# Kernel optimization log

Measured on AMD Instinct MI355X. Metric: run time of the kernel, lower is better.

## Reference

```python
import jax, jax.numpy as jnp
import numpy as np

EMBED_DIM = 1024
NUM_HEADS = 16
HEAD_DIM = EMBED_DIM // NUM_HEADS
LN_EPS = 1e-5


def setup_inputs() -> dict:
    key = jax.random.key(0)
    ks = jax.random.split(key, 5)
    N, L, C = 32, 577, EMBED_DIM
    x = jax.random.normal(ks[0], (N, L, C), dtype=jnp.float32)
    ln1_g = jnp.ones((C,), dtype=jnp.float32)
    ln1_b = jnp.zeros((C,), dtype=jnp.float32)
    w_in = jax.random.normal(ks[1], (3 * C, C), dtype=jnp.float32) * (C ** -0.5)
    b_in = jax.random.normal(ks[2], (3 * C,), dtype=jnp.float32) * 0.02
    w_out = jax.random.normal(ks[3], (C, C), dtype=jnp.float32) * (C ** -0.5)
    b_out = jax.random.normal(ks[4], (C,), dtype=jnp.float32) * 0.02
    return {"x": x, "ln1_g": ln1_g, "ln1_b": ln1_b, "w_in": w_in,
            "b_in": b_in, "w_out": w_out, "b_out": b_out}


def _layernorm(x, g, b):
    mu = jnp.mean(x, axis=-1, keepdims=True)
    var = jnp.mean(jnp.square(x - mu), axis=-1, keepdims=True)
    return (x - mu) * jax.lax.rsqrt(var + LN_EPS) * g + b


def reference(x, ln1_g, ln1_b, w_in, b_in, w_out, b_out):
    # ClearCLIP last block, attn_variant='qq', keep_residual=False, keep_ffn=False.
    N, L, C = x.shape
    H, D = NUM_HEADS, HEAD_DIM
    z = _layernorm(x, ln1_g, ln1_b)
    qkv = z @ w_in.T + b_in                      # (N, L, 3C)
    q, k, v = jnp.split(qkv, 3, axis=-1)
    k = q                                        # 'qq' self-self variant
    def heads(t):
        return t.reshape(N, L, H, D).transpose(0, 2, 1, 3)  # (N, H, L, D)
    q, k, v = heads(q), heads(k), heads(v)
    scale = 1.0 / np.sqrt(D).astype(np.float32)
    scores = jnp.einsum('nhld,nhsd->nhls', q, k) * scale    # (N, H, L, L)
    attn = jax.nn.softmax(scores, axis=-1)
    out = jnp.einsum('nhls,nhsd->nhld', attn, v)            # (N, H, L, D)
    out = out.transpose(0, 2, 1, 3).reshape(N, L, C)
    return out @ w_out.T + b_out                 # ls_1 = Identity, no residual/FFN
```

## Files before the change

### kernel.cpp

```cpp
#include <hip/hip_runtime.h>
#include <stdint.h>

typedef short bf16x8 __attribute__((ext_vector_type(8)));
typedef float f32x4 __attribute__((ext_vector_type(4)));
typedef unsigned int uint4v __attribute__((ext_vector_type(4)));
typedef unsigned short ushort4v __attribute__((ext_vector_type(4)));
typedef float float4v __attribute__((ext_vector_type(4)));

#define MROWS 18464
#define SEQ   577
#define CDIM  1024
#define SPAD  640
#define W1ELEMS (2048*1024)
#define W2ELEMS (1024*1024)
#define SQC 0.42466089f

__device__ __forceinline__ unsigned short f2bf(float f) {
  unsigned int u = __float_as_uint(f);
  u += 0x7fffu + ((u >> 16) & 1u);
  return (unsigned short)(u >> 16);
}

__device__ __forceinline__ void load_lds16(const void* g, void* lds) {
  __builtin_amdgcn_global_load_lds(
      (const __attribute__((address_space(1))) unsigned int*)(uint64_t)(uintptr_t)g,
      (__attribute__((address_space(3))) unsigned int*)(unsigned int)(uintptr_t)lds,
      16, 0, 0);
}

__global__ __launch_bounds__(256) void ln_kernel(const float* __restrict__ x,
                                                 const float* __restrict__ g,
                                                 const float* __restrict__ b,
                                                 unsigned short* __restrict__ z) {
  const int row = blockIdx.x;
  const int t = threadIdx.x;
  const float4v v = *(const float4v*)(x + (size_t)row * CDIM + t * 4);
  float s  = v[0] + v[1] + v[2] + v[3];
  float ss = v[0]*v[0] + v[1]*v[1] + v[2]*v[2] + v[3]*v[3];
  #pragma unroll
  for (int off = 1; off < 64; off <<= 1) { s += __shfl_xor(s, off); ss += __shfl_xor(ss, off); }
  __shared__ float rs[4], rss[4];
  const int w = t >> 6, l = t & 63;
  if (l == 0) { rs[w] = s; rss[w] = ss; }
  __syncthreads();
  s = rs[0] + rs[1] + rs[2] + rs[3];
  ss = rss[0] + rss[1] + rss[2] + rss[3];
  const float mu = s * (1.0f / CDIM);
  const float var = ss * (1.0f / CDIM) - mu * mu;
  const float rstd = rsqrtf(var + 1e-5f);
  const float4v gv = *(const float4v*)(g + t * 4);
  const float4v bv = *(const float4v*)(b + t * 4);
  ushort4v o;
  #pragma unroll
  for (int j = 0; j < 4; ++j) o[j] = f2bf((v[j] - mu) * rstd * gv[j] + bv[j]);
  *(ushort4v*)(z + (size_t)row * CDIM + t * 4) = o;
}

__global__ __launch_bounds__(256) void conv_kernel(const float* __restrict__ w_in,
                                                   const float* __restrict__ w_out,
                                                   unsigned short* __restrict__ wqv,
                                                   unsigned short* __restrict__ wo,
                                                   unsigned short* __restrict__ vt) {
  const int idx = blockIdx.x * 256 + threadIdx.x;
  const int e = idx * 4;
  if (e < W1ELEMS) {
    const int row = e >> 10;
    const int srow = row < 1024 ? row : row + 1024;
    const float4v v = *(const float4v*)(w_in + (size_t)srow * 1024 + (e & 1023));
    ushort4v o;
    #pragma unroll
    for (int j = 0; j < 4; ++j) o[j] = f2bf(v[j]);
    *(ushort4v*)(wqv + e) = o;
  } else if (e < W1ELEMS + W2ELEMS) {
    const int e2 = e - W1ELEMS;
    const float4v v = *(const float4v*)(w_out + e2);
    ushort4v o;
    #pragma unroll
    for (int j = 0; j < 4; ++j) o[j] = f2bf(v[j]);
    *(ushort4v*)(wo + e2) = o;
  } else {
    const int pidx = idx - (W1ELEMS + W2ELEMS) / 4;
    const int ic = pidx >> 3, part = pidx & 7;
    *(uint4v*)(vt + (size_t)ic * SPAD + 576 + part * 8) = (uint4v)0u;
  }
}

__global__ __launch_bounds__(1024, 4) void gemm_qv(const unsigned short* __restrict__ A,
                                                   const unsigned short* __restrict__ B,
                                                   const float* __restrict__ bias,
                                                   unsigned short* __restrict__ qout,
                                                   unsigned short* __restrict__ vtout) {
  __shared__ char smem[131072];
  const int t = threadIdx.x;
  const int w = t >> 6, l = t & 63;
  const int L = (blockIdx.x & 7) * 73 + (blockIdx.x >> 3);
  const int p = L >> 3, c = L & 7;
  const int m0 = p * 256, n0 = c * 256;
  const int wm = w >> 2, wn = w & 3;
  const int g4 = (l >> 4) * 4;
  const int fr = l & 15;
  const int fb = (l >> 4) * 16;
  const int sw = (l & 7) << 4;

  f32x4 acc[4][4];
  #pragma unroll
  for (int i = 0; i < 4; ++i)
    #pragma unroll
    for (int j = 0; j < 4; ++j) acc[i][j] = (f32x4)0.0f;

  const int srow = l >> 3;
  const int scol = ((((l & 7) * 16) ^ ((srow & 7) << 4)) >> 1);
  int ra0 = m0 + w * 16 + srow;     if (ra0 > MROWS - 1) ra0 = MROWS - 1;
  int ra1 = m0 + w * 16 + 8 + srow; if (ra1 > MROWS - 1) ra1 = MROWS - 1;
  const unsigned short* pA0 = A + (size_t)ra0 * 1024 + scol;
  const unsigned short* pA1 = A + (size_t)ra1 * 1024 + scol;
  const unsigned short* pB0 = B + (size_t)(n0 + w * 16 + srow) * 1024 + scol;
  const unsigned short* pB1 = pB0 + (size_t)8 * 1024;

  #define STG(kt, buf)                                                     \
    {                                                                      \
      char* const dA_ = smem + (buf) * 65536 + w * 2048;                   \
      char* const dB_ = dA_ + 32768;                                       \
      const int k0_ = (kt) * 64;                                           \
      load_lds16(pA0 + k0_, dA_);                                          \
      load_lds16(pA1 + k0_, dA_ + 1024);                                   \
      load_lds16(pB0 + k0_, dB_);                                          \
      load_lds16(pB1 + k0_, dB_ + 1024);                                   \
    }

  STG(0, 0)
  __syncthreads();

  for (int kb = 0; kb < 16; ++kb) {
    const int b = kb & 1;
    if (kb < 15) STG(kb + 1, b ^ 1)
    const char* Ab = smem + b * 65536;
    const char* Bb = Ab + 32768;
    #pragma unroll
    for (int kk = 0; kk < 2; ++kk) {
      bf16x8 af[4], bfr[4];
      #pragma unroll
      for (int i = 0; i < 4; ++i)
        af[i] = *(const bf16x8*)(Ab + (wm * 64 + i * 16 + fr) * 128 + ((kk * 64 + fb) ^ sw));
      #pragma unroll
      for (int j = 0; j < 4; ++j)
        bfr[j] = *(const bf16x8*)(Bb + (wn * 64 + j * 16 + fr) * 128 + ((kk * 64 + fb) ^ sw));
      #pragma unroll
      for (int i = 0; i < 4; ++i)
        #pragma unroll
        for (int j = 0; j < 4; ++j)
          acc[i][j] = __builtin_amdgcn_mfma_f32_16x16x32_bf16(af[i], bfr[j], acc[i][j], 0, 0, 0);
    }
    __syncthreads();
  }
  #undef STG

  unsigned short* sm = (unsigned short*)smem;
  const bool isq = (n0 < 1024);
  const float* bb = isq ? (bias + n0) : (bias + 1024 + n0);
  const float scl = isq ? SQC : 1.0f;
  float bcol[4];
  #pragma unroll
  for (int j = 0; j < 4; ++j) bcol[j] = bb[wn * 64 + j * 16 + fr];
  for (int pass = 0; pass < 4; ++pass) {
    if (wm == pass) {
      #pragma unroll
      for (int i = 0; i < 4; ++i)
        #pragma unroll
        for (int j = 0; j < 4; ++j)
          #pragma unroll
          for (int r = 0; r < 4; ++r)
            sm[(i * 16 + g4 + r) * 264 + wn * 64 + j * 16 + fr] =
                f2bf((acc[i][j][r] + bcol[j]) * scl);
    }
    __syncthreads();
    if (isq) {
      #pragma unroll
      for (int it = 0; it < 2; ++it) {
        const int cid = it * 1024 + t;
        const int row = cid >> 5, ch = cid & 31;
        const int grow = m0 + pass * 64 + row;
        if (grow < MROWS)
          *(uint4v*)(qout + (size_t)grow * 1024 + n0 + ch * 8) =
              *(const uint4v*)(sm + row * 264 + ch * 8);
      }
    } else {
      const int tokloc = t & 63, chgrp = t >> 6;
      const int token = m0 + pass * 64 + tokloc;
      if (token < MROWS) {
        const unsigned int nimg = (unsigned int)token / 577u;
        const int s = token - (int)(nimg * 577u);
        unsigned short* op =
            vtout + ((size_t)nimg * 1024 + (n0 - 1024) + chgrp * 16) * SPAD + s;
        const unsigned short* sp = sm + tokloc * 264 + chgrp * 16;
        #pragma unroll 8
        for (int it = 0; it < 16; ++it)
          op[(size_t)it * SPAD] = sp[it];
      }
    }
    __syncthreads();
  }
}

__global__ __launch_bounds__(1024, 4) void gemm_proj(const unsigned short* __restrict__ A,
                                                     const unsigned short* __restrict__ B,
                                                     const float* __restrict__ bias,
                                                     float* __restrict__ outp) {
  __shared__ char smem[98304];
  const int t = threadIdx.x;
  const int w = t >> 6, l = t & 63;
  const int L = (blockIdx.x & 7) * 73 + (blockIdx.x >> 3);
  const int p = L >> 3, c = L & 7;
  const int m0 = p * 256, n0 = c * 128;
  const int wm = w >> 2, wn = w & 3;
  const int g4 = (l >> 4) * 4;
  const int fr = l & 15;
  const int fb = (l >> 4) * 16;
  const int sw = (l & 7) << 4;

  f32x4 acc[4][2];
  #pragma unroll
  for (int i = 0; i < 4; ++i)
    #pragma unroll
    for (int j = 0; j < 2; ++j) acc[i][j] = (f32x4)0.0f;

  const int srow = l >> 3;
  const int scol = ((((l & 7) * 16) ^ ((srow & 7) << 4)) >> 1);
  int ra0 = m0 + w * 16 + srow;     if (ra0 > MROWS - 1) ra0 = MROWS - 1;
  int ra1 = m0 + w * 16 + 8 + srow; if (ra1 > MROWS - 1) ra1 = MROWS - 1;
  const unsigned short* pA0 = A + (size_t)ra0 * 1024 + scol;
  const unsigned short* pA1 = A + (size_t)ra1 * 1024 + scol;
  const unsigned short* pB0 = B + (size_t)(n0 + w * 8 + srow) * 1024 + scol;

  #define STG(kt, buf)                                                     \
    {                                                                      \
      char* const dA_ = smem + (buf) * 49152 + w * 2048;                   \
      const int k0_ = (kt) * 64;                                           \
      load_lds16(pA0 + k0_, dA_);                                          \
      load_lds16(pA1 + k0_, dA_ + 1024);                                   \
      load_lds16(pB0 + k0_, smem + (buf) * 49152 + 32768 + w * 1024);      \
    }

  STG(0, 0)
  __syncthreads();

  for (int kb = 0; kb < 16; ++kb) {
    const int b = kb & 1;
    if (kb < 15) STG(kb + 1, b ^ 1)
    const char* Ab = smem + b * 49152;
    const char* Bb = Ab + 32768;
    #pragma unroll
    for (int kk = 0; kk < 2; ++kk) {
      bf16x8 af[4], bfr[2];
      #pragma unroll
      for (int i = 0; i < 4; ++i)
        af[i] = *(const bf16x8*)(Ab + (wm * 64 + i * 16 + fr) * 128 + ((kk * 64 + fb) ^ sw));
      #pragma unroll
      for (int j = 0; j < 2; ++j)
        bfr[j] = *(const bf16x8*)(Bb + (wn * 32 + j * 16 + fr) * 128 + ((kk * 64 + fb) ^ sw));
      #pragma unroll
      for (int i = 0; i < 4; ++i)
        #pragma unroll
        for (int j = 0; j < 2; ++j)
          acc[i][j] = __builtin_amdgcn_mfma_f32_16x16x32_bf16(af[i], bfr[j], acc[i][j], 0, 0, 0);
    }
    __syncthreads();
  }
  #undef STG

  float* smf = (float*)smem;
  float bcol[2];
  #pragma unroll
  for (int j = 0; j < 2; ++j) bcol[j] = bias[n0 + wn * 32 + j * 16 + fr];
  for (int q8 = 0; q8 < 8; ++q8) {
    if (wm == (q8 >> 1)) {
      const int i0 = (q8 & 1) * 2;
      #pragma unroll
      for (int i2 = 0; i2 < 2; ++i2)
        #pragma unroll
        for (int j = 0; j < 2; ++j)
          #pragma unroll
          for (int r = 0; r < 4; ++r)
            smf[(i2 * 16 + g4 + r) * 132 + wn * 32 + j * 16 + fr] =
                acc[i0 + i2][j][r] + bcol[j];
    }
    __syncthreads();
    {
      const int row = t >> 5, ch = t & 31;
      const int grow = m0 + q8 * 32 + row;
      if (grow < MROWS)
        *(float4v*)(outp + (size_t)grow * 1024 + n0 + ch * 4) =
            *(const float4v*)(smf + row * 132 + ch * 4);
    }
    __syncthreads();
  }
}

__global__ __launch_bounds__(256) void attn_kernel(const unsigned short* __restrict__ qbuf,
                                                   const unsigned short* __restrict__ vt,
                                                   unsigned short* __restrict__ out) {
  __shared__ char smem[32768];
  const int t = threadIdx.x, w = t >> 6, l = t & 63;
  const int g = l >> 4, fr = l & 15;
  const int bid = blockIdx.x;
  const int xcd = bid & 7, idx = bid >> 3;
  const int nhl = idx / 5;
  const int qb = idx - nhl * 5;
  const int nh = xcd * 64 + nhl;
  const int n = nh >> 4, h = nh & 15;
  const size_t rowbase = (size_t)n * SEQ;
  const int sw = (l & 7) << 4;

  bf16x8 bq[2][2];
  #pragma unroll
  for (int half = 0; half < 2; ++half) {
    const unsigned short* qp =
        qbuf + (rowbase + qb * 128 + half * 64 + w * 16 + fr) * 1024 + h * 64 + g * 8;
    bq[half][0] = *(const bf16x8*)qp;
    bq[half][1] = *(const bf16x8*)(qp + 32);
  }

  const int srow = l >> 3;
  const int scolE = ((((l & 7) * 16) ^ ((srow & 7) << 4)) >> 1);
  const unsigned short* ksrc = qbuf + (rowbase + w * 16 + srow) * 1024 + h * 64 + scolE;
  const unsigned short* vsrc = vt + ((size_t)nh * 64 + w * 16 + srow) * SPAD + scolE;

  f32x4 acc[2][4];
  #pragma unroll
  for (int half = 0; half < 2; ++half)
    #pragma unroll
    for (int cf = 0; cf < 4; ++cf) acc[half][cf] = (f32x4)0.0f;
  float l_run[2] = {0.0f, 0.0f};

  {
    char* kdst = smem + (w * 16) * 128;
    char* vdst = smem + 8192 + (w * 16) * 128;
    load_lds16(ksrc, kdst);
    load_lds16(ksrc + (size_t)8 * 1024, kdst + 1024);
    load_lds16(vsrc, vdst);
    load_lds16(vsrc + 8 * SPAD, vdst + 1024);
  }
  __syncthreads();

  for (int kb = 0; kb < 10; ++kb) {
    const int b = kb & 1;
    const char* kbuf = smem + b * 16384;
    const char* vbuf = kbuf + 8192;

    if (kb < 9) {
      char* kdst = smem + (b ^ 1) * 16384 + (w * 16) * 128;
      char* vdst = kdst + 8192;
      load_lds16(ksrc + (size_t)((kb + 1) * 64) * 1024, kdst);
      load_lds16(ksrc + (size_t)((kb + 1) * 64 + 8) * 1024, kdst + 1024);
      load_lds16(vsrc + (kb + 1) * 64, vdst);
      load_lds16(vsrc + 8 * SPAD + (kb + 1) * 64, vdst + 1024);
    }

    f32x4 s4[2][4];
    #pragma unroll
    for (int half = 0; half < 2; ++half)
      #pragma unroll
      for (int cf = 0; cf < 4; ++cf) s4[half][cf] = (f32x4)0.0f;
    #pragma unroll
    for (int kk = 0; kk < 2; ++kk)
      #pragma unroll
      for (int cf = 0; cf < 4; ++cf) {
        const bf16x8 af = *(const bf16x8*)(kbuf + (cf * 16 + fr) * 128 + ((kk * 64 + g * 16) ^ sw));
        s4[0][cf] = __builtin_amdgcn_mfma_f32_16x16x32_bf16(af, bq[0][kk], s4[0][cf], 0, 0, 0);
        s4[1][cf] = __builtin_amdgcn_mfma_f32_16x16x32_bf16(af, bq[1][kk], s4[1][cf], 0, 0, 0);
      }

    if (kb == 9) {
      #pragma unroll
      for (int half = 0; half < 2; ++half) {
        #pragma unroll
        for (int cf = 0; cf < 4; ++cf)
          #pragma unroll
          for (int r = 0; r < 4; ++r)
            if (cf != 0 || r != 0) s4[half][cf][r] = -__builtin_inff();
        s4[half][0][0] = (g == 0) ? s4[half][0][0] : -__builtin_inff();
      }
    }

    bf16x8 ap[2][2];
    #pragma unroll
    for (int half = 0; half < 2; ++half) {
      float sum = 0.0f;
      #pragma unroll
      for (int cf = 0; cf < 4; ++cf)
        #pragma unroll
        for (int r = 0; r < 4; ++r) {
          const float p2 = __builtin_amdgcn_exp2f(s4[half][cf][r]);
          s4[half][cf][r] = p2;
          sum += p2;
        }
      sum += __shfl_xor(sum, 16);
      sum += __shfl_xor(sum, 32);
      l_run[half] += sum;

      unsigned int pka[4], pkb[4];
      #pragma unroll
      for (int cf = 0; cf < 4; ++cf) {
        asm("v_cvt_pk_bf16_f32 %0, %1, %2" : "=v"(pka[cf]) : "v"(s4[half][cf][0]), "v"(s4[half][cf][1]));
        asm("v_cvt_pk_bf16_f32 %0, %1, %2" : "=v"(pkb[cf]) : "v"(s4[half][cf][2]), "v"(s4[half][cf][3]));
      }
      #pragma unroll
      for (int kk = 0; kk < 2; ++kk) {
        unsigned int a0 = pka[2 * kk], b0 = pka[2 * kk + 1];
        unsigned int a1 = pkb[2 * kk], b1 = pkb[2 * kk + 1];
        asm("v_permlane32_swap_b32 %0, %1" : "+v"(a0), "+v"(b0));
        asm("v_permlane16_swap_b32 %0, %1" : "+v"(a0), "+v"(b0));
        asm("v_permlane32_swap_b32 %0, %1" : "+v"(a1), "+v"(b1));
        asm("v_permlane16_swap_b32 %0, %1" : "+v"(a1), "+v"(b1));
        union { unsigned int i[4]; bf16x8 v; } u;
        u.i[0] = a0; u.i[1] = a1; u.i[2] = b0; u.i[3] = b1;
        ap[half][kk] = u.v;
      }
    }

    #pragma unroll
    for (int kk = 0; kk < 2; ++kk)
      #pragma unroll
      for (int cf = 0; cf < 4; ++cf) {
        const bf16x8 bv = *(const bf16x8*)(vbuf + (cf * 16 + fr) * 128 + ((kk * 64 + g * 16) ^ sw));
        acc[0][cf] = __builtin_amdgcn_mfma_f32_16x16x32_bf16(ap[0][kk], bv, acc[0][cf], 0, 0, 0);
        acc[1][cf] = __builtin_amdgcn_mfma_f32_16x16x32_bf16(ap[1][kk], bv, acc[1][cf], 0, 0, 0);
      }

    __syncthreads();
  }

  #pragma unroll
  for (int half = 0; half < 2; ++half) {
    const float rcp = 1.0f / l_run[half];
    #pragma unroll
    for (int r = 0; r < 4; ++r) {
      const float rr = __shfl(rcp, g * 4 + r);
      const int qg = qb * 128 + half * 64 + w * 16 + g * 4 + r;
      if (qg < SEQ) {
        #pragma unroll
        for (int cf = 0; cf < 4; ++cf)
          out[(rowbase + qg) * 1024 + h * 64 + cf * 16 + fr] = f2bf(acc[half][cf][r] * rr);
      }
    }
  }
}

extern "C" void kernel_launch(void* const* d_in, const int* in_sizes, int n_in,
                              void* d_out, int out_size, void* d_ws, size_t ws_size,
                              hipStream_t stream) {
  const float* x     = (const float*)d_in[0];
  const float* ln_g  = (const float*)d_in[1];
  const float* ln_b  = (const float*)d_in[2];
  const float* w_in  = (const float*)d_in[3];
  const float* b_in  = (const float*)d_in[4];
  const float* w_out = (const float*)d_in[5];
  const float* b_out = (const float*)d_in[6];

  unsigned short* z    = (unsigned short*)d_ws;
  unsigned short* qbuf = z + (size_t)MROWS * 1024;
  unsigned short* vt   = qbuf + (size_t)MROWS * 1024;
  unsigned short* wqv  = vt + (size_t)512 * 64 * SPAD;
  unsigned short* wo   = wqv + (size_t)2048 * 1024;

  ln_kernel<<<MROWS, 256, 0, stream>>>(x, ln_g, ln_b, z);
  conv_kernel<<<4096, 256, 0, stream>>>(w_in, w_out, wqv, wo, vt);
  gemm_qv<<<584, 1024, 0, stream>>>(z, wqv, b_in, qbuf, vt);
  attn_kernel<<<2560, 256, 0, stream>>>(qbuf, vt, z);
  gemm_proj<<<584, 1024, 0, stream>>>(z, wo, b_out, (float*)d_out);
}
```

Baseline: 243.4 us.

## Use 2-wave attention blocks with 64 query rows per wave and MFMA priority

The attention kernel drops from 4 to 2 waves per block. Each wave now handles 64 query rows (four 16-row groups) instead of 32, so every K/V fragment read from LDS feeds twice as many MFMAs, and each wave stages twice as many K/V rows per tile. The P·V step is interleaved per 16-row group, and the MFMA sections are wrapped in s_setprio raises. The cost is higher register pressure from 4x4 accumulators and score tiles, plus fewer waves per block to hide latency.

Measured after the change: 271.3 us. 11.5% more time.

```diff
diff --git a/kernel.cpp b/kernel.cpp
--- a/kernel.cpp
+++ b/kernel.cpp
@@ -296,7 +296,7 @@
   }
 }
 
-__global__ __launch_bounds__(256) void attn_kernel(const unsigned short* __restrict__ qbuf,
+__global__ __launch_bounds__(128) void attn_kernel(const unsigned short* __restrict__ qbuf,
                                                    const unsigned short* __restrict__ vt,
                                                    unsigned short* __restrict__ out) {
   __shared__ char smem[32768];
@@ -311,35 +311,39 @@
   const size_t rowbase = (size_t)n * SEQ;
   const int sw = (l & 7) << 4;
 
-  bf16x8 bq[2][2];
-  #pragma unroll
-  for (int half = 0; half < 2; ++half) {
+  bf16x8 bq[4][2];
+  #pragma unroll
+  for (int h2 = 0; h2 < 4; ++h2) {
     const unsigned short* qp =
-        qbuf + (rowbase + qb * 128 + half * 64 + w * 16 + fr) * 1024 + h * 64 + g * 8;
-    bq[half][0] = *(const bf16x8*)qp;
-    bq[half][1] = *(const bf16x8*)(qp + 32);
+        qbuf + (rowbase + qb * 128 + w * 64 + h2 * 16 + fr) * 1024 + h * 64 + g * 8;
+    bq[h2][0] = *(const bf16x8*)qp;
+    bq[h2][1] = *(const bf16x8*)(qp + 32);
   }
 
   const int srow = l >> 3;
   const int scolE = ((((l & 7) * 16) ^ ((srow & 7) << 4)) >> 1);
-  const unsigned short* ksrc = qbuf + (rowbase + w * 16 + srow) * 1024 + h * 64 + scolE;
-  const unsigned short* vsrc = vt + ((size_t)nh * 64 + w * 16 + srow) * SPAD + scolE;
-
-  f32x4 acc[2][4];
-  #pragma unroll
-  for (int half = 0; half < 2; ++half)
-    #pragma unroll
-    for (int cf = 0; cf < 4; ++cf) acc[half][cf] = (f32x4)0.0f;
-  float l_run[2] = {0.0f, 0.0f};
-
-  {
-    char* kdst = smem + (w * 16) * 128;
-    char* vdst = smem + 8192 + (w * 16) * 128;
-    load_lds16(ksrc, kdst);
-    load_lds16(ksrc + (size_t)8 * 1024, kdst + 1024);
-    load_lds16(vsrc, vdst);
-    load_lds16(vsrc + 8 * SPAD, vdst + 1024);
-  }
+  const unsigned short* ksrc = qbuf + (rowbase + w * 32 + srow) * 1024 + h * 64 + scolE;
+  const unsigned short* vsrc = vt + ((size_t)nh * 64 + w * 32 + srow) * SPAD + scolE;
+
+  f32x4 acc[4][4];
+  #pragma unroll
+  for (int h2 = 0; h2 < 4; ++h2)
+    #pragma unroll
+    for (int cf = 0; cf < 4; ++cf) acc[h2][cf] = (f32x4)0.0f;
+  float l_run[4] = {0.0f, 0.0f, 0.0f, 0.0f};
+
+  #define ASTG(kb_, buf_)                                                          \
+    {                                                                              \
+      char* kdst = smem + (buf_) * 16384 + (w * 32) * 128;                         \
+      char* vdst = kdst + 8192;                                                    \
+      _Pragma("unroll")                                                            \
+      for (int c2 = 0; c2 < 4; ++c2) {                                             \
+        load_lds16(ksrc + (size_t)((kb_) * 64 + c2 * 8) * 1024, kdst + c2 * 1024); \
+        load_lds16(vsrc + c2 * 8 * SPAD + (kb_) * 64, vdst + c2 * 1024);           \
+      }                                                                            \
+    }
+
+  ASTG(0, 0)
   __syncthreads();
 
   for (int kb = 0; kb < 10; ++kb) {
@@ -347,63 +351,59 @@
     const char* kbuf = smem + b * 16384;
     const char* vbuf = kbuf + 8192;
 
-    if (kb < 9) {
-      char* kdst = smem + (b ^ 1) * 16384 + (w * 16) * 128;
-      char* vdst = kdst + 8192;
-      load_lds16(ksrc + (size_t)((kb + 1) * 64) * 1024, kdst);
-      load_lds16(ksrc + (size_t)((kb + 1) * 64 + 8) * 1024, kdst + 1024);
-      load_lds16(vsrc + (kb + 1) * 64, vdst);
-      load_lds16(vsrc + 8 * SPAD + (kb + 1) * 64, vdst + 1024);
-    }
-
-    f32x4 s4[2][4];
-    #pragma unroll
-    for (int half = 0; half < 2; ++half)
-      #pragma unroll
-      for (int cf = 0; cf < 4; ++cf) s4[half][cf] = (f32x4)0.0f;
+    if (kb < 9) ASTG(kb + 1, b ^ 1)
+
+    f32x4 s4[4][4];
+    #pragma unroll
+    for (int h2 = 0; h2 < 4; ++h2)
+      #pragma unroll
+      for (int cf = 0; cf < 4; ++cf) s4[h2][cf] = (f32x4)0.0f;
+    __builtin_amdgcn_s_setprio(1);
     #pragma unroll
     for (int kk = 0; kk < 2; ++kk)
       #pragma unroll
       for (int cf = 0; cf < 4; ++cf) {
         const bf16x8 af = *(const bf16x8*)(kbuf + (cf * 16 + fr) * 128 + ((kk * 64 + g * 16) ^ sw));
-        s4[0][cf] = __builtin_amdgcn_mfma_f32_16x16x32_bf16(af, bq[0][kk], s4[0][cf], 0, 0, 0);
-        s4[1][cf] = __builtin_amdgcn_mfma_f32_16x16x32_bf16(af, bq[1][kk], s4[1][cf], 0, 0, 0);
-      }
+        #pragma unroll
+        for (int h2 = 0; h2 < 4; ++h2)
+          s4[h2][cf] = __builtin_amdgcn_mfma_f32_16x16x32_bf16(af, bq[h2][kk], s4[h2][cf], 0, 0, 0);
+      }
+    __builtin_amdgcn_s_setprio(0);
 
     if (kb == 9) {
       #pragma unroll
-      for (int half = 0; half < 2; ++half) {
+      for (int h2 = 0; h2 < 4; ++h2) {
         #pragma unroll
         for (int cf = 0; cf < 4; ++cf)
           #pragma unroll
           for (int r = 0; r < 4; ++r)
-            if (cf != 0 || r != 0) s4[half][cf][r] = -__builtin_inff();
-        s4[half][0][0] = (g == 0) ? s4[half][0][0] : -__builtin_inff();
-      }
-    }
-
-    bf16x8 ap[2][2];
-    #pragma unroll
-    for (int half = 0; half < 2; ++half) {
+            if (cf != 0 || r != 0) s4[h2][cf][r] = -__builtin_inff();
+        s4[h2][0][0] = (g == 0) ? s4[h2][0][0] : -__builtin_inff();
+      }
+    }
+
+    #pragma unroll
+    for (int h2 = 0; h2 < 4; ++h2) {
       float sum = 0.0f;
       #pragma unroll
       for (int cf = 0; cf < 4; ++cf)
         #pragma unroll
         for (int r = 0; r < 4; ++r) {
-          const float p2 = __builtin_amdgcn_exp2f(s4[half][cf][r]);
-          s4[half][cf][r] = p2;
+          const float p2 = __builtin_amdgcn_exp2f(s4[h2][cf][r]);
+          s4[h2][cf][r] = p2;
           sum += p2;
         }
       sum += __shfl_xor(sum, 16);
       sum += __shfl_xor(sum, 32);
-      l_run[half] += sum;
+      l_run[h2] += sum;
 
       unsigned int pka[4], pkb[4];
       #pragma unroll
       for (int cf = 0; cf < 4; ++cf) {
-        asm("v_cvt_pk_bf16_f32 %0, %1, %2" : "=v"(pka[cf]) : "v"(s4[half][cf][0]), "v"(s4[half][cf][1]));
-        asm("v_cvt_pk_bf16_f32 %0, %1, %2" : "=v"(pkb[cf]) : "v"(s4[half][cf][2]), "v"(s4[half][cf][3]));
-      }
+        asm("v_cvt_pk_bf16_f32 %0, %1, %2" : "=v"(pka[cf]) : "v"(s4[h2][cf][0]), "v"(s4[h2][cf][1]));
+        asm("v_cvt_pk_bf16_f32 %0, %1, %2" : "=v"(pkb[cf]) : "v"(s4[h2][cf][2]), "v"(s4[h2][cf][3]));
+      }
+      bf16x8 ap[2];
       #pragma unroll
       for (int kk = 0; kk < 2; ++kk) {
         unsigned int a0 = pka[2 * kk], b0 = pka[2 * kk + 1];
@@ -414,33 +414,34 @@
         asm("v_permlane16_swap_b32 %0, %1" : "+v"(a1), "+v"(b1));
         union { unsigned int i[4]; bf16x8 v; } u;
         u.i[0] = a0; u.i[1] = a1; u.i[2] = b0; u.i[3] = b1;
-        ap[half][kk] = u.v;
-      }
-    }
-
-    #pragma unroll
-    for (int kk = 0; kk < 2; ++kk)
-      #pragma unroll
-      for (int cf = 0; cf < 4; ++cf) {
-        const bf16x8 bv = *(const bf16x8*)(vbuf + (cf * 16 + fr) * 128 + ((kk * 64 + g * 16) ^ sw));
-        acc[0][cf] = __builtin_amdgcn_mfma_f32_16x16x32_bf16(ap[0][kk], bv, acc[0][cf], 0, 0, 0);
-        acc[1][cf] = __builtin_amdgcn_mfma_f32_16x16x32_bf16(ap[1][kk], bv, acc[1][cf], 0, 0, 0);
-      }
-
-    __syncthreads();
-  }
-
-  #pragma unroll
-  for (int half = 0; half < 2; ++half) {
-    const float rcp = 1.0f / l_run[half];
+        ap[kk] = u.v;
+      }
+      __builtin_amdgcn_s_setprio(1);
+      #pragma unroll
+      for (int kk = 0; kk < 2; ++kk)
+        #pragma unroll
+        for (int cf = 0; cf < 4; ++cf) {
+          const bf16x8 bv = *(const bf16x8*)(vbuf + (cf * 16 + fr) * 128 + ((kk * 64 + g * 16) ^ sw));
+          acc[h2][cf] = __builtin_amdgcn_mfma_f32_16x16x32_bf16(ap[kk], bv, acc[h2][cf], 0, 0, 0);
+        }
+      __builtin_amdgcn_s_setprio(0);
+    }
+
+    __syncthreads();
+  }
+  #undef ASTG
+
+  #pragma unroll
+  for (int h2 = 0; h2 < 4; ++h2) {
+    const float rcp = 1.0f / l_run[h2];
     #pragma unroll
     for (int r = 0; r < 4; ++r) {
       const float rr = __shfl(rcp, g * 4 + r);
-      const int qg = qb * 128 + half * 64 + w * 16 + g * 4 + r;
+      const int qg = qb * 128 + w * 64 + h2 * 16 + g * 4 + r;
       if (qg < SEQ) {
         #pragma unroll
         for (int cf = 0; cf < 4; ++cf)
-          out[(rowbase + qg) * 1024 + h * 64 + cf * 16 + fr] = f2bf(acc[half][cf][r] * rr);
+          out[(rowbase + qg) * 1024 + h * 64 + cf * 16 + fr] = f2bf(acc[h2][cf][r] * rr);
       }
     }
   }
@@ -466,6 +467,6 @@
   ln_kernel<<<MROWS, 256, 0, stream>>>(x, ln_g, ln_b, z);
   conv_kernel<<<4096, 256, 0, stream>>>(w_in, w_out, wqv, wo, vt);
   gemm_qv<<<584, 1024, 0, stream>>>(z, wqv, b_in, qbuf, vt);
-  attn_kernel<<<2560, 256, 0, stream>>>(qbuf, vt, z);
+  attn_kernel<<<2560, 128, 0, stream>>>(qbuf, vt, z);
   gemm_proj<<<584, 1024, 0, stream>>>(z, wo, b_out, (float*)d_out);
 }
```
